# Kernel tuning notes

Measured on AMD Instinct MI355X. Metric: run time of the kernel, lower is better.

## Reference

```python
import jax, jax.numpy as jnp
import numpy as np

B = 1024
IN_SHAPE = ((8, 8, 8), (8, 8))
IN_RANKS = ((32, 32, 32), (32, 32))
OUT_SHAPE = (16, 16, 16)
OUT_RANK = (32, 32, 32)


def _xavier(key, shape):
    # xavier_normal over axes [0,1] (in) and [2] (out), matching the torch helper
    fan_in = shape[0] * shape[1]
    fan_out = shape[2]
    std = float(np.sqrt(2.0 / (fan_in + fan_out)))
    return jax.random.normal(key, shape, dtype=jnp.float32) * std


def setup_inputs() -> dict:
    key = jax.random.key(0)
    ks = jax.random.split(key, 12)
    x_dims = tuple(d for g in IN_SHAPE for d in g)
    inp = {"x": jax.random.normal(ks[0], (B,) + x_dims, dtype=jnp.float32)}
    # input TT factors, flattened over groups in order (group, mode)
    fac_shapes = []
    for shapes, ranks in zip(IN_SHAPE, IN_RANKS):
        for i in range(len(shapes)):
            r_prev = 1 if i == 0 else ranks[i - 1]
            fac_shapes.append((r_prev, shapes[i], ranks[i]))
    for idx, fs in enumerate(fac_shapes):
        inp[f"f{idx}"] = _xavier(ks[1 + idx], fs)
    # core: (last rank of each group..., output_rank[-1])
    core_shape = tuple(r[-1] for r in IN_RANKS) + (OUT_RANK[-1],)
    fan_in = int(np.prod(core_shape[:-1]))
    std = float(np.sqrt(2.0 / (fan_in + core_shape[-1])))
    inp["core"] = jax.random.normal(ks[6], core_shape, dtype=jnp.float32) * std
    # output TT factors
    for i in range(len(OUT_SHAPE)):
        r_prev = 1 if i == 0 else OUT_RANK[i - 1]
        inp[f"g{i}"] = _xavier(ks[7 + i], (r_prev, OUT_SHAPE[i], OUT_RANK[i]))
    # bias: uniform(-1/sqrt(fan_in), +) with fan_in = total input features
    total_in = int(np.prod([np.prod(s) for s in IN_SHAPE]))
    bound = 1.0 / float(np.sqrt(total_in))
    inp["bias"] = jax.random.uniform(ks[10], OUT_SHAPE, dtype=jnp.float32,
                                     minval=-bound, maxval=bound)
    return inp


def reference(x, f0, f1, f2, f3, f4, core, g0, g1, g2, bias):
    groups = ((f0, f1, f2), (f3, f4))
    Bsz = x.shape[0]
    # T: [B, remaining_modes_flat, accumulated_group_ranks_flat]
    T = x.reshape(Bsz, -1)[:, :, None]
    for facs in groups:
        first = facs[0][0]                       # squeeze dummy rank-1: [n, r]
        n = first.shape[0]
        T = T.reshape(Bsz, n, -1, T.shape[-1])   # [B, n, M', Racc]
        T = jnp.einsum("bnmq,nr->bmqr", T, first)  # [B, M', Racc, r]
        for f in facs[1:]:
            n = f.shape[1]
            T = T.reshape(Bsz, n, -1, T.shape[-2], T.shape[-1])
            T = jnp.einsum("bnmqp,pnr->bmqr", T, f)
        # fold this group's final rank into the accumulated rank axis
        T = T.reshape(Bsz, T.shape[1], -1)
    # all input modes consumed -> T is [B, 1, r1_last*r2_last]
    z = T.reshape(Bsz, -1) @ core.reshape(-1, core.shape[-1])  # [B, Rout]
    # output TT chain -> W[o0, o1, o2, R_last]
    W = g0[0]
    for g in (g1, g2):
        W = jnp.einsum("...p,poq->...oq", W, g)
    R = W.shape[-1]
    out = z @ W.reshape(-1, R).T                 # [B, prod(OUT_SHAPE)]
    out = out.reshape((Bsz,) + OUT_SHAPE)
    return out + bias
```

## Files before the change

### kernel.cpp

```cpp
#include <hip/hip_runtime.h>
#include <stdint.h>

#define WS_M2 0
#define WS_N2 16384
#define WS_WT 18432
#define WS_Z  149504

#define GLOAD_LDS16(gsrc, ldst)                                         \
    __builtin_amdgcn_global_load_lds(                                   \
        (const __attribute__((address_space(1))) uint32_t*)(gsrc),      \
        (__attribute__((address_space(3))) uint32_t*)(ldst), 16, 0, 0)

#define FMA4(A, X, mm) do { (A).x += (X).x*(mm); (A).y += (X).y*(mm); \
                            (A).z += (X).z*(mm); (A).w += (X).w*(mm); } while (0)

__global__ __launch_bounds__(256) void precompute_kernel(
    const float* __restrict__ f0, const float* __restrict__ f1,
    const float* __restrict__ f2, const float* __restrict__ f3,
    const float* __restrict__ f4, const float* __restrict__ g0,
    const float* __restrict__ g1, const float* __restrict__ g2,
    float* __restrict__ ws)
{
    __shared__ float sA[8192];
    const int t = threadIdx.x;
    const int blk = blockIdx.x;
    if (blk < 8) {
        for (int i = t; i < 2048; i += 256) {
            int a01 = i >> 5, r2 = i & 31;
            int a0 = a01 >> 3, a1 = a01 & 7;
            float s = 0.f;
            #pragma unroll
            for (int r1 = 0; r1 < 32; ++r1)
                s += f0[a0*32 + r1] * f1[r1*256 + a1*32 + r2];
            sA[i] = s;
        }
        __syncthreads();
        for (int i = t; i < 2048; i += 256) {
            int a012 = blk*64 + (i >> 5), r3 = i & 31;
            int a01 = a012 >> 3, a2 = a012 & 7;
            float s = 0.f;
            #pragma unroll
            for (int r2 = 0; r2 < 32; ++r2)
                s += sA[a01*32 + r2] * f2[r2*256 + a2*32 + r3];
            ws[WS_M2 + a012*32 + r3] = s;
        }
    } else if (blk == 8) {
        for (int i = t; i < 2048; i += 256) {
            int a34 = i >> 5, s2 = i & 31;
            int a3 = a34 >> 3, a4 = a34 & 7;
            float s = 0.f;
            #pragma unroll
            for (int s1 = 0; s1 < 32; ++s1)
                s += f3[a3*32 + s1] * f4[s1*256 + a4*32 + s2];
            ws[WS_N2 + i] = s;
        }
    } else {
        const int j = blk - 9;
        for (int i = t; i < 8192; i += 256) {
            int o01 = i >> 5, q = i & 31;
            int o0 = o01 >> 4, o1 = o01 & 15;
            float s = 0.f;
            #pragma unroll
            for (int p = 0; p < 32; ++p)
                s += g0[o0*32 + p] * g1[p*512 + o1*32 + q];
            sA[i] = s;
        }
        __syncthreads();
        for (int i = t; i < 4096; i += 256) {
            int o = j*128 + (i >> 5);
            int r = i & 31;
            int o01 = o >> 4, o2 = o & 15;
            float s = 0.f;
            #pragma unroll
            for (int q = 0; q < 32; ++q)
                s += sA[o01*32 + q] * g2[q*512 + o2*32 + r];
            ws[WS_WT + r*4096 + o] = s;
        }
    }
}

__global__ __launch_bounds__(256, 4) void main_kernel(
    const float* __restrict__ x, const float* __restrict__ core,
    const float* __restrict__ ws, float* __restrict__ zout)
{
    __shared__ float s[10240];
    const int t = threadIdx.x;
    const int b = blockIdx.x;
    const int w    = __builtin_amdgcn_readfirstlane(t >> 6);
    const int lane = t & 63;
    const int tm = lane & 7;
    const int tr = lane >> 3;

    float* __restrict__ R = s + w*2048;
    const float* __restrict__ xg = x + (size_t)b*32768 + w*8192;
    const float* __restrict__ mg = ws + WS_M2 + w*4096;

    GLOAD_LDS16(xg + lane*4,        R);
    GLOAD_LDS16(xg + 256 + lane*4,  R + 256);
    GLOAD_LDS16(mg + lane*4,        R + 1024);

    float4 accA[4], accB[4];
    #pragma unroll
    for (int rr = 0; rr < 4; ++rr) {
        accA[rr].x = accA[rr].y = accA[rr].z = accA[rr].w = 0.f;
        accB[rr].x = accB[rr].y = accB[rr].z = accB[rr].w = 0.f;
    }

    #pragma unroll 1
    for (int c = 0; c < 16; ++c) {
        if (c < 15) {
            const float* sx = xg + (c+1)*512 + lane*4;
            float* dx = R + ((c+1)&1)*512;
            GLOAD_LDS16(sx,       dx);
            GLOAD_LDS16(sx + 256, dx + 256);
            GLOAD_LDS16(mg + (c+1)*256 + lane*4, R + 1024 + ((c+1)&1)*256);
            asm volatile("s_waitcnt vmcnt(3)" ::: "memory");
        } else {
            const float* sn = ws + WS_N2 + w*512 + lane*4;
            GLOAD_LDS16(sn,       s + 8192 + w*512);
            GLOAD_LDS16(sn + 256, s + 8192 + w*512 + 256);
            asm volatile("s_waitcnt vmcnt(2)" ::: "memory");
        }
        const float* __restrict__ xt = R + (c&1)*512 + tm*8;
        const float* __restrict__ mt = R + 1024 + (c&1)*256 + tr*4;
        #pragma unroll
        for (int kk = 0; kk < 8; ++kk) {
            float4 xlo = *(const float4*)(xt + kk*64);
            float4 xhi = *(const float4*)(xt + kk*64 + 4);
            float4 m4  = *(const float4*)(mt + kk*32);
            FMA4(accA[0], xlo, m4.x); FMA4(accB[0], xhi, m4.x);
            FMA4(accA[1], xlo, m4.y); FMA4(accB[1], xhi, m4.y);
            FMA4(accA[2], xlo, m4.z); FMA4(accB[2], xhi, m4.z);
            FMA4(accA[3], xlo, m4.w); FMA4(accB[3], xhi, m4.w);
        }
    }

    #pragma unroll
    for (int rr = 0; rr < 4; ++rr) {
        const int r = tr*4 + rr;
        float* d = R + r*64 + ((tm ^ (r & 7)) << 3);
        d[0]=accA[rr].x; d[1]=accA[rr].y; d[2]=accA[rr].z; d[3]=accA[rr].w;
        d[4]=accB[rr].x; d[5]=accB[rr].y; d[6]=accB[rr].z; d[7]=accB[rr].w;
    }
    __syncthreads();

    {
        const int rr = t >> 3;
        const int mo = t & 7;
        const int off = rr*64 + (((mo ^ (rr & 7))) << 3);
        float sm[8];
        #pragma unroll
        for (int i = 0; i < 8; ++i)
            sm[i] = s[off + i] + s[2048 + off + i]
                  + s[4096 + off + i] + s[6144 + off + i];
        #pragma unroll
        for (int i = 0; i < 8; ++i) s[off + i] = sm[i];
    }
    __syncthreads();

    {
        const int r3  = t >> 3;
        const int s2b = (t & 7) * 4;
        float a0=0.f, a1=0.f, a2=0.f, a3=0.f;
        #pragma unroll 8
        for (int m = 0; m < 64; ++m) {
            float av = s[r3*64 + (((m >> 3) ^ (r3 & 7)) << 3) + (m & 7)];
            const float* n = &s[8192 + m*32 + s2b];
            a0 += av*n[0]; a1 += av*n[1]; a2 += av*n[2]; a3 += av*n[3];
        }
        float* d = &s[2048 + r3*32 + s2b];
        d[0]=a0; d[1]=a1; d[2]=a2; d[3]=a3;
    }
    __syncthreads();

    {
        const int ro2 = t & 15;
        const int kc  = t >> 4;
        const float2* core2 = (const float2*)core;
        float s0 = 0.f, s1 = 0.f;
        const int k0 = kc * 64;
        for (int k = k0; k < k0 + 64; ++k) {
            float tv = s[2048 + k];
            float2 cv = core2[k*16 + ro2];
            s0 += tv*cv.x; s1 += tv*cv.y;
        }
        s[3072 + kc*32 + ro2*2 + 0] = s0;
        s[3072 + kc*32 + ro2*2 + 1] = s1;
    }
    __syncthreads();
    if (t < 32) {
        float acc = 0.f;
        #pragma unroll
        for (int kc = 0; kc < 16; ++kc) acc += s[3072 + kc*32 + t];
        zout[b*32 + t] = acc;
    }
}

__global__ __launch_bounds__(256) void out_kernel(
    const float* __restrict__ ws, const float* __restrict__ bias,
    float* __restrict__ out)
{
    __shared__ float sW[8192];
    __shared__ float sZt[2176];
    __shared__ float sB[256];
    const int t  = threadIdx.x;
    const int bt = blockIdx.x;
    const int ot = blockIdx.y;

    {
        const float4* wt4 = (const float4*)(ws + WS_WT);
        float4* d = (float4*)sW;
        #pragma unroll
        for (int i = 0; i < 8; ++i) {
            int idx = i*256 + t;
            int ro = idx >> 6, oc = idx & 63;
            d[idx] = wt4[ro*1024 + ot*64 + oc];
        }
    }
    {
        const float4* z4 = (const float4*)(ws + WS_Z) + bt*512;
        #pragma unroll
        for (int i = 0; i < 2; ++i) {
            int idx = i*256 + t;
            int bl = idx >> 3, r4 = idx & 7;
            float4 v = z4[idx];
            sZt[(r4*4 + 0)*68 + bl] = v.x;
            sZt[(r4*4 + 1)*68 + bl] = v.y;
            sZt[(r4*4 + 2)*68 + bl] = v.z;
            sZt[(r4*4 + 3)*68 + bl] = v.w;
        }
    }
    if (t < 64) {
        const float4* b4 = (const float4*)bias + ot*64;
        ((float4*)sB)[t] = b4[t];
    }
    __syncthreads();

    const int oc = t & 63;
    const int bg = t >> 6;
    const float4* sW4 = (const float4*)sW;
    const float4 bv = ((const float4*)sB)[oc];
    float4* out4 = (float4*)out;

    for (int bi = 0; bi < 16; bi += 4) {
        const int bl = bg*16 + bi;
        float4 a0 = bv, a1 = bv, a2 = bv, a3 = bv;
        #pragma unroll
        for (int ro = 0; ro < 32; ++ro) {
            float4 w = sW4[ro*64 + oc];
            float4 z = *(const float4*)&sZt[ro*68 + bl];
            a0.x += z.x*w.x; a0.y += z.x*w.y; a0.z += z.x*w.z; a0.w += z.x*w.w;
            a1.x += z.y*w.x; a1.y += z.y*w.y; a1.z += z.y*w.z; a1.w += z.y*w.w;
            a2.x += z.z*w.x; a2.y += z.z*w.y; a2.z += z.z*w.z; a2.w += z.z*w.w;
            a3.x += z.w*w.x; a3.y += z.w*w.y; a3.z += z.w*w.z; a3.w += z.w*w.w;
        }
        const size_t obase = (size_t)(bt*64 + bl) * 1024 + ot*64 + oc;
        out4[obase + 0*1024] = a0;
        out4[obase + 1*1024] = a1;
        out4[obase + 2*1024] = a2;
        out4[obase + 3*1024] = a3;
    }
}

extern "C" void kernel_launch(void* const* d_in, const int* in_sizes, int n_in,
                              void* d_out, int out_size, void* d_ws, size_t ws_size,
                              hipStream_t stream)
{
    const float* x    = (const float*)d_in[0];
    const float* f0   = (const float*)d_in[1];
    const float* f1   = (const float*)d_in[2];
    const float* f2   = (const float*)d_in[3];
    const float* f3   = (const float*)d_in[4];
    const float* f4   = (const float*)d_in[5];
    const float* core = (const float*)d_in[6];
    const float* g0   = (const float*)d_in[7];
    const float* g1   = (const float*)d_in[8];
    const float* g2   = (const float*)d_in[9];
    const float* bias = (const float*)d_in[10];
    float* ws  = (float*)d_ws;
    float* out = (float*)d_out;

    precompute_kernel<<<41, 256, 0, stream>>>(f0, f1, f2, f3, f4, g0, g1, g2, ws);
    main_kernel<<<1024, 256, 0, stream>>>(x, core, ws, ws + WS_Z);
    out_kernel<<<dim3(16, 16), 256, 0, stream>>>(ws, bias, out);
}
```

Before: 265.2 us.

## Deepen main_kernel LDS prefetch pipeline from double to quad buffering

Switches the per-wave x/M2 staging from two LDS buffers to four, keeping three chunks of global->LDS loads in flight with matching vmcnt waits, so more memory latency is hidden. The N2 load moves out of the main loop and now overlaps with the cross-wave reduction. The later stages are relocated in LDS, with a padded stride on the intermediate, to fit the new layout. LDS per block grows and the launch-bounds occupancy hint drops from 4 to 3 blocks, which may reduce latency hiding across blocks.

```diff
diff --git a/kernel.cpp b/kernel.cpp
--- a/kernel.cpp
+++ b/kernel.cpp
@@ -79,11 +79,11 @@
     }
 }
 
-__global__ __launch_bounds__(256, 4) void main_kernel(
+__global__ __launch_bounds__(256, 3) void main_kernel(
     const float* __restrict__ x, const float* __restrict__ core,
     const float* __restrict__ ws, float* __restrict__ zout)
 {
-    __shared__ float s[10240];
+    __shared__ float s[12288];
     const int t = threadIdx.x;
     const int b = blockIdx.x;
     const int w    = __builtin_amdgcn_readfirstlane(t >> 6);
@@ -91,13 +91,16 @@
     const int tm = lane & 7;
     const int tr = lane >> 3;
 
-    float* __restrict__ R = s + w*2048;
+    float* __restrict__ R = s + w*3072;
     const float* __restrict__ xg = x + (size_t)b*32768 + w*8192;
     const float* __restrict__ mg = ws + WS_M2 + w*4096;
 
-    GLOAD_LDS16(xg + lane*4,        R);
-    GLOAD_LDS16(xg + 256 + lane*4,  R + 256);
-    GLOAD_LDS16(mg + lane*4,        R + 1024);
+    #pragma unroll
+    for (int j = 0; j < 3; ++j) {
+        GLOAD_LDS16(xg + j*512 + lane*4,       R + j*512);
+        GLOAD_LDS16(xg + j*512 + 256 + lane*4, R + j*512 + 256);
+        GLOAD_LDS16(mg + j*256 + lane*4,       R + 2048 + j*256);
+    }
 
     float4 accA[4], accB[4];
     #pragma unroll
@@ -108,21 +111,23 @@
 
     #pragma unroll 1
     for (int c = 0; c < 16; ++c) {
-        if (c < 15) {
-            const float* sx = xg + (c+1)*512 + lane*4;
-            float* dx = R + ((c+1)&1)*512;
+        if (c < 13) {
+            const int d = c + 3;
+            const float* sx = xg + d*512 + lane*4;
+            float* dx = R + (d&3)*512;
             GLOAD_LDS16(sx,       dx);
             GLOAD_LDS16(sx + 256, dx + 256);
-            GLOAD_LDS16(mg + (c+1)*256 + lane*4, R + 1024 + ((c+1)&1)*256);
+            GLOAD_LDS16(mg + d*256 + lane*4, R + 2048 + (d&3)*256);
+            asm volatile("s_waitcnt vmcnt(9)" ::: "memory");
+        } else if (c == 13) {
+            asm volatile("s_waitcnt vmcnt(6)" ::: "memory");
+        } else if (c == 14) {
             asm volatile("s_waitcnt vmcnt(3)" ::: "memory");
         } else {
-            const float* sn = ws + WS_N2 + w*512 + lane*4;
-            GLOAD_LDS16(sn,       s + 8192 + w*512);
-            GLOAD_LDS16(sn + 256, s + 8192 + w*512 + 256);
-            asm volatile("s_waitcnt vmcnt(2)" ::: "memory");
-        }
-        const float* __restrict__ xt = R + (c&1)*512 + tm*8;
-        const float* __restrict__ mt = R + 1024 + (c&1)*256 + tr*4;
+            asm volatile("s_waitcnt vmcnt(0)" ::: "memory");
+        }
+        const float* __restrict__ xt = R + (c&3)*512 + tm*8;
+        const float* __restrict__ mt = R + 2048 + (c&3)*256 + tr*4;
         #pragma unroll
         for (int kk = 0; kk < 8; ++kk) {
             float4 xlo = *(const float4*)(xt + kk*64);
@@ -145,17 +150,24 @@
     __syncthreads();
 
     {
+        const float* sn = ws + WS_N2 + w*512 + lane*4;
+        GLOAD_LDS16(sn,       R + 2048);
+        GLOAD_LDS16(sn + 256, R + 2048 + 256);
+    }
+
+    {
         const int rr = t >> 3;
         const int mo = t & 7;
-        const int off = rr*64 + (((mo ^ (rr & 7))) << 3);
+        const int off = rr*64 + ((mo ^ (rr & 7)) << 3);
         float sm[8];
         #pragma unroll
         for (int i = 0; i < 8; ++i)
-            sm[i] = s[off + i] + s[2048 + off + i]
-                  + s[4096 + off + i] + s[6144 + off + i];
+            sm[i] = s[off + i] + s[3072 + off + i]
+                  + s[6144 + off + i] + s[9216 + off + i];
         #pragma unroll
         for (int i = 0; i < 8; ++i) s[off + i] = sm[i];
     }
+    asm volatile("s_waitcnt vmcnt(0)" ::: "memory");
     __syncthreads();
 
     {
@@ -165,10 +177,10 @@
         #pragma unroll 8
         for (int m = 0; m < 64; ++m) {
             float av = s[r3*64 + (((m >> 3) ^ (r3 & 7)) << 3) + (m & 7)];
-            const float* n = &s[8192 + m*32 + s2b];
+            const float* n = &s[(m >> 4)*3072 + 2048 + (m & 15)*32 + s2b];
             a0 += av*n[0]; a1 += av*n[1]; a2 += av*n[2]; a3 += av*n[3];
         }
-        float* d = &s[2048 + r3*32 + s2b];
+        float* d = &s[3072 + r3*36 + s2b];
         d[0]=a0; d[1]=a1; d[2]=a2; d[3]=a3;
     }
     __syncthreads();
@@ -180,18 +192,18 @@
         float s0 = 0.f, s1 = 0.f;
         const int k0 = kc * 64;
         for (int k = k0; k < k0 + 64; ++k) {
-            float tv = s[2048 + k];
+            float tv = s[3072 + (k >> 5)*36 + (k & 31)];
             float2 cv = core2[k*16 + ro2];
             s0 += tv*cv.x; s1 += tv*cv.y;
         }
-        s[3072 + kc*32 + ro2*2 + 0] = s0;
-        s[3072 + kc*32 + ro2*2 + 1] = s1;
+        s[6144 + kc*32 + ro2*2 + 0] = s0;
+        s[6144 + kc*32 + ro2*2 + 1] = s1;
     }
     __syncthreads();
     if (t < 32) {
         float acc = 0.f;
         #pragma unroll
-        for (int kc = 0; kc < 16; ++kc) acc += s[3072 + kc*32 + t];
+        for (int kc = 0; kc < 16; ++kc) acc += s[6144 + kc*32 + t];
         zout[b*32 + t] = acc;
     }
 }
```

After: 301.8 us. 13.8% more time.
